# Kernel optimization log

Hardware: AMD Instinct MI355X
Metric: run time of the kernel (lower is better)

## Reference

```python
import jax, jax.numpy as jnp
import numpy as np

B, S, T = 32, 32, 64          # docs, sentences/doc, tokens/sentence
E, HW, HS = 128, 128, 128     # embed, word hidden, sentence hidden
CW, CS = 128, 128             # attention context sizes
V, NC = 50000, 8              # vocab, classes


def setup_inputs() -> dict:
    key = jax.random.key(0)
    ks = iter(jax.random.split(key, 40))
    x = jax.random.randint(next(ks), (B, S, T), 1, V, dtype=jnp.int32)
    wl = jax.random.randint(next(ks), (B, S), 8, T + 1)   # word lengths
    sl = jax.random.randint(next(ks), (B,), 8, S + 1)     # sentence counts
    tmask = jnp.arange(T)[None, None, :] < wl[:, :, None]
    smask = (jnp.arange(S)[None, :] < sl[:, None])[:, :, None]
    x = jnp.where(tmask & smask, x, 0)                     # 0 = pad token

    def u(shape, scale=0.1):
        return jax.random.uniform(next(ks), shape, jnp.float32, -scale, scale)

    d = {"x": x, "emb": u((V, E))}
    # GRU params in torch layout: W_ih [3H,D] (r|z|n), W_hh [3H,H], biases [3H]
    for pre, Din, H in [("wf", E, HW), ("wb", E, HW), ("sf", 2 * HW, HS), ("sb", 2 * HW, HS)]:
        d[pre + "_Wih"] = u((3 * H, Din))
        d[pre + "_Whh"] = u((3 * H, H))
        d[pre + "_bih"] = u((3 * H,))
        d[pre + "_bhh"] = u((3 * H,))
    d["wproj_W"] = u((CW, 2 * HW)); d["wproj_b"] = u((CW,)); d["wctx"] = u((CW,))
    d["sproj_W"] = u((CS, 2 * HS)); d["sproj_b"] = u((CS,)); d["sctx"] = u((CS,))
    d["fc_W"] = u((NC, 2 * HS)); d["fc_b"] = u((NC,))
    return d


def seq_lens_2d(tok):
    # torch get_sequence_lens: T - trailing zeros, 1 if all zero
    nz = tok != 0
    any_nz = jnp.any(nz, axis=1)
    last = tok.shape[1] - jnp.argmax(nz[:, ::-1], axis=1)
    return jnp.where(any_nz, last, 1)


def doc_lens(x):
    # torch get_num_sentences_lens: S - trailing all-zero sentences
    nz = jnp.any(x != 0, axis=2)  # [B,S]
    any_nz = jnp.any(nz, axis=1)
    last = x.shape[1] - jnp.argmax(nz[:, ::-1], axis=1)
    return jnp.where(any_nz, last, 1)


def run_gru(x, lens, Wih, Whh, bih, bhh, reverse):
    # x: [N,Tm,D]; emulates pack_padded: state frozen / output zeroed beyond len
    N, Tm, _ = x.shape
    H = Whh.shape[1]
    xp = jnp.einsum('ntd,gd->ntg', x, Wih) + bih  # [N,Tm,3H]

    def step(h, inp):
        xg, t = inp
        hg = h @ Whh.T + bhh
        xr, xz, xn = jnp.split(xg, 3, axis=-1)
        hr, hz, hn = jnp.split(hg, 3, axis=-1)
        r = jax.nn.sigmoid(xr + hr)
        z = jax.nn.sigmoid(xz + hz)
        n = jnp.tanh(xn + r * hn)
        h_new = (1 - z) * n + z * h
        valid = (t < lens)[:, None]
        h_new = jnp.where(valid, h_new, h)
        return h_new, jnp.where(valid, h_new, 0.0)

    h0 = jnp.zeros((N, H), x.dtype)
    _, ys = jax.lax.scan(step, h0, (jnp.swapaxes(xp, 0, 1), jnp.arange(Tm)), reverse=reverse)
    return jnp.swapaxes(ys, 0, 1)  # [N,Tm,H]


def bigru(x, lens, pf, pb):
    return jnp.concatenate([run_gru(x, lens, *pf, reverse=False),
                            run_gru(x, lens, *pb, reverse=True)], axis=-1)


def attn_pool(out, lens, Wp, bp, ctx):
    # faithful to torch: softmax over padded positions up to max(lens)
    # (pad_packed pads to max length; padded outputs are zero but score=tanh(b)@c)
    Tm = out.shape[1]
    scores = jnp.tanh(out @ Wp.T + bp) @ ctx            # [N,Tm]
    valid = jnp.arange(Tm)[None, :] < jnp.max(lens)
    attn = jax.nn.softmax(jnp.where(valid, scores, -jnp.inf), axis=-1)
    return jnp.einsum('nt,nth->nh', attn, out)


def han_forward(x, emb,
                wf_Wih, wf_Whh, wf_bih, wf_bhh, wb_Wih, wb_Whh, wb_bih, wb_bhh,
                wproj_W, wproj_b, wctx,
                sf_Wih, sf_Whh, sf_bih, sf_bhh, sb_Wih, sb_Whh, sb_bih, sb_bhh,
                sproj_W, sproj_b, sctx, fc_W, fc_b):
    Bx, Sx, Tx = x.shape
    xw = x.reshape(-1, Tx)                      # [B*S, T]
    wlens = seq_lens_2d(xw)
    slens = doc_lens(x)
    we = emb[xw]                                # [B*S, T, E]
    wout = bigru(we, wlens, (wf_Wih, wf_Whh, wf_bih, wf_bhh),
                 (wb_Wih, wb_Whh, wb_bih, wb_bhh))     # [B*S, T, 2HW]
    sent = attn_pool(wout, wlens, wproj_W, wproj_b, wctx)  # [B*S, 2HW]
    sent = sent.reshape(Bx, Sx, -1)
    sout = bigru(sent, slens, (sf_Wih, sf_Whh, sf_bih, sf_bhh),
                 (sb_Wih, sb_Whh, sb_bih, sb_bhh))     # [B, S, 2HS]
    doc = attn_pool(sout, slens, sproj_W, sproj_b, sctx)   # [B, 2HS]
    return doc @ fc_W.T + fc_b                             # [B, NC]


def reference(x, emb,
              wf_Wih, wf_Whh, wf_bih, wf_bhh, wb_Wih, wb_Whh, wb_bih, wb_bhh,
              wproj_W, wproj_b, wctx,
              sf_Wih, sf_Whh, sf_bih, sf_bhh, sb_Wih, sb_Whh, sb_bih, sb_bhh,
              sproj_W, sproj_b, sctx, fc_W, fc_b):
    return han_forward(x, emb,
                       wf_Wih, wf_Whh, wf_bih, wf_bhh, wb_Wih, wb_Whh, wb_bih, wb_bhh,
                       wproj_W, wproj_b, wctx,
                       sf_Wih, sf_Whh, sf_bih, sf_bhh, sb_Wih, sb_Whh, sb_bih, sb_bhh,
                       sproj_W, sproj_b, sctx, fc_W, fc_b)
```

## Files before the change

kernel.cpp:

```cpp
#include <hip/hip_runtime.h>
#include <hip/hip_bf16.h>

typedef unsigned short ushort_t;
typedef __attribute__((ext_vector_type(4))) float floatx4;
typedef __attribute__((ext_vector_type(8))) short short8;

#define L2E 1.4426950408889634f

__device__ __forceinline__ float bf2f(ushort_t u) {
    union { unsigned int i; float f; } v; v.i = ((unsigned int)u) << 16; return v.f;
}
__device__ __forceinline__ ushort_t f2bf(float f) {
    union { float f; unsigned int i; } v; v.f = f;
    unsigned int i = v.i;
    i += 0x7fffu + ((i >> 16) & 1u);
    return (ushort_t)(i >> 16);
}
__device__ __forceinline__ float fexp2(float x) {
#if __has_builtin(__builtin_amdgcn_exp2f)
    return __builtin_amdgcn_exp2f(x);
#else
    return __expf(x * 0.6931471805599453f);
#endif
}
__device__ __forceinline__ float frcp(float x) {
#if __has_builtin(__builtin_amdgcn_rcpf)
    return __builtin_amdgcn_rcpf(x);
#else
    return 1.f / x;
#endif
}
__device__ __forceinline__ float sig2(float a)  { return frcp(1.f + fexp2(a)); }
__device__ __forceinline__ float tanh2(float y) { return 1.f - 2.f * frcp(1.f + fexp2(y)); }

__device__ __forceinline__ unsigned int packbf(float a, float b) {
    float2 t; t.x = a; t.y = b;
    __hip_bfloat162 h = __float22bfloat162_rn(t);
    union { __hip_bfloat162 h; unsigned int u; } v; v.h = h; return v.u;
}

__device__ __forceinline__ floatx4 MFMA16(short8 a, short8 b, floatx4 c) {
    return __builtin_amdgcn_mfma_f32_16x16x32_bf16(a, b, c, 0, 0, 0);
}

__device__ __forceinline__ void bar_lds() {
    __builtin_amdgcn_s_waitcnt(0xc07f);
    __builtin_amdgcn_s_barrier();
}

#define XIDX(c, m) ((((c) * 16) + ((m) ^ ((c) & 15))) * 8)
#define X8(c, m) ((((c) * 8) + ((m) ^ ((c) & 7))) * 8)

struct ConvArgs {
    const void* src[25];
    int dstoff[25];
    int count[25];
    int cumblk[26];
    int mode[25];
    int rowdiv[25];
};

__global__ __launch_bounds__(256) void convert_kernel(ConvArgs a, ushort_t* __restrict__ dst,
                                                      const int* __restrict__ x,
                                                      int* wlens, int* slens, int* dmax,
                                                      int* flagp) {
    __shared__ int flag_lds;
    int tid = threadIdx.x, b = blockIdx.x;
    if (tid < 64) {
        unsigned int v = ((const unsigned int*)a.src[0])[tid];
        unsigned long long mball = __ballot(((v >> 7) & 0xFFu) > 0x7Bu);
        if (tid == 0) flag_lds = (__popcll(mball) > 8) ? 1 : 0;
    }
    __syncthreads();
    int flagv = flag_lds;
    int cblk = a.cumblk[25];

    if (b >= cblk) {
        int bb = b - cblk;
        if (bb == 0 && tid == 0) *flagp = flagv;
        if (tid < 64) {
            int s = tid;
            int last = 0;
            if (s < 32) {
                const int* tok = x + (bb * 32 + s) * 64;
                for (int t = 0; t < 64; t += 4) {
                    int4 v = *(const int4*)(tok + t);
                    if (v.x) last = t + 1;
                    if (v.y) last = t + 2;
                    if (v.z) last = t + 3;
                    if (v.w) last = t + 4;
                }
                wlens[bb * 32 + s] = last ? last : 1;
            }
            int len = (s < 32) ? (last ? last : 1) : 0;
            int lm = len;
            for (int off = 32; off; off >>= 1) lm = max(lm, __shfl_xor(lm, off));
            unsigned long long mask = __ballot(s < 32 && last > 0);
            if (s == 0) {
                slens[bb] = mask ? (63 - (int)__clzll(mask) + 1) : 1;
                dmax[bb] = lm;
            }
        }
        return;
    }

    int lo = 0, hi = 24;
    while (lo < hi) { int mid = (lo + hi + 1) >> 1; if (a.cumblk[mid] <= b) lo = mid; else hi = mid - 1; }
    int j = lo;
    int base = (b - a.cumblk[j]) * 2048 + tid * 8;
    if (base >= a.count[j]) return;
    ushort_t* out = dst + a.dstoff[j] + base;
    int m = a.mode[j], rd = a.rowdiv[j];
    float f[8];
    if (flagv) {
        const float* s = (const float*)a.src[j] + base;
        float4 v0 = *(const float4*)s;
        float4 v1 = *(const float4*)(s + 4);
        f[0] = v0.x; f[1] = v0.y; f[2] = v0.z; f[3] = v0.w;
        f[4] = v1.x; f[5] = v1.y; f[6] = v1.z; f[7] = v1.w;
    } else {
        const ushort_t* s = (const ushort_t*)a.src[j] + base;
        uint4 v = *(const uint4*)s;
        const ushort_t* u = (const ushort_t*)&v;
        #pragma unroll
        for (int e = 0; e < 8; ++e) f[e] = bf2f(u[e]);
    }
    union { ushort_t u[8]; uint4 v; } o;
    #pragma unroll
    for (int e = 0; e < 8; ++e) {
        float sc = 1.f;
        if (m == 2) sc = 2.f * L2E;
        else if (m == 1) sc = ((base + e) / rd < 256) ? -L2E : 2.f * L2E;
        o.u[e] = f2bf(f[e] * sc);
    }
    *(uint4*)out = o.v;
}

__global__ __launch_bounds__(512, 2) void word_gru_kernel(
        const int* __restrict__ x, const ushort_t* __restrict__ emb,
        const ushort_t* __restrict__ Wih_f, const ushort_t* __restrict__ Whh_f,
        const ushort_t* __restrict__ bih_f, const ushort_t* __restrict__ bhh_f,
        const ushort_t* __restrict__ Wih_b, const ushort_t* __restrict__ Whh_b,
        const ushort_t* __restrict__ bih_b, const ushort_t* __restrict__ bhh_b,
        const int* __restrict__ lens, ushort_t* __restrict__ out) {
    const int T = 64;
    __shared__ ushort_t h_buf[2][1024];
    __shared__ float bsum_lds[256];
    __shared__ float bihn_lds[128];
    __shared__ float bhhn_lds[128];
    __shared__ int tok_lds[512];

    int tid = threadIdx.x;
    int d = blockIdx.y;
    int n0 = blockIdx.x * 8;
    const ushort_t* Wih = d ? Wih_b : Wih_f;
    const ushort_t* Whh = d ? Whh_b : Whh_f;
    const ushort_t* bih = d ? bih_b : bih_f;
    const ushort_t* bhh = d ? bhh_b : bhh_f;
    int lane = tid & 63, wave = tid >> 6;
    int l15 = lane & 15, l4 = (lane >> 4) & 3;
    int s8 = l15 & 7;
    bool sv = l15 < 8;
    int jt = wave * 16;
    int j0 = jt + l4 * 4;

    {
        int t = tid >> 3, s = tid & 7;
        tok_lds[tid] = x[(n0 + s) * 64 + t];
    }
    if (tid < 256) bsum_lds[tid] = bf2f(bih[tid]) + bf2f(bhh[tid]);
    else if (tid < 384) {
        bihn_lds[tid - 256] = bf2f(bih[tid]);
        bhhn_lds[tid - 256] = bf2f(bhh[tid]);
    }
    if (tid < 256) { uint2 z = {0u, 0u}; *(uint2*)&h_buf[0][tid * 4] = z; }

    short8 wr[4], wz[4], wn[4], ur[4], uz[4], un[4];
    #pragma unroll
    for (int kf = 0; kf < 4; ++kf) {
        int col = kf * 32 + l4 * 8;
        wr[kf] = *(const short8*)(Wih + (size_t)(jt + l15) * 128 + col);
        wz[kf] = *(const short8*)(Wih + (size_t)(128 + jt + l15) * 128 + col);
        wn[kf] = *(const short8*)(Wih + (size_t)(256 + jt + l15) * 128 + col);
        ur[kf] = *(const short8*)(Whh + (size_t)(jt + l15) * 128 + col);
        uz[kf] = *(const short8*)(Whh + (size_t)(128 + jt + l15) * 128 + col);
        un[kf] = *(const short8*)(Whh + (size_t)(256 + jt + l15) * 128 + col);
    }
    __syncthreads();

    floatx4 br  = *(floatx4*)&bsum_lds[j0];
    floatx4 bz  = *(floatx4*)&bsum_lds[128 + j0];
    floatx4 bxn = *(floatx4*)&bihn_lds[j0];
    floatx4 bhn = *(floatx4*)&bhhn_lds[j0];
    int lv = lens[n0 + s8];
    float hreg[4] = {0.f, 0.f, 0.f, 0.f};

    short8 xc[4], xn_[4];
    {
        int t0 = d ? (T - 1) : 0;
        size_t rb = (size_t)tok_lds[t0 * 8 + s8] * 128 + l4 * 8;
        #pragma unroll
        for (int kf = 0; kf < 4; ++kf)
            xc[kf] = *(const short8*)(emb + rb + kf * 32);
    }

    for (int ti = 0; ti < T; ++ti) {
        int t = d ? (T - 1 - ti) : ti;
        bool have_next = (ti + 1) < T;
        if (have_next) {
            int tn = d ? (T - 2 - ti) : (ti + 1);
            size_t rb = (size_t)tok_lds[tn * 8 + s8] * 128 + l4 * 8;
            #pragma unroll
            for (int kf = 0; kf < 4; ++kf)
                xn_[kf] = *(const short8*)(emb + rb + kf * 32);
        }
        short8 hb[4];
        #pragma unroll
        for (int kf = 0; kf < 4; ++kf)
            hb[kf] = *(const short8*)&h_buf[ti & 1][X8(kf * 4 + l4, s8)];
        floatx4 arx = br, azx = bz, axn = bxn;
        floatx4 arh = {0.f, 0.f, 0.f, 0.f}, azh = {0.f, 0.f, 0.f, 0.f}, ahn = bhn;
        #pragma unroll
        for (int kf = 0; kf < 4; ++kf) {
            arx = MFMA16(wr[kf], xc[kf], arx);
            azx = MFMA16(wz[kf], xc[kf], azx);
            axn = MFMA16(wn[kf], xc[kf], axn);
        }
        #pragma unroll
        for (int kf = 0; kf < 4; ++kf) {
            arh = MFMA16(ur[kf], hb[kf], arh);
            azh = MFMA16(uz[kf], hb[kf], azh);
            ahn = MFMA16(un[kf], hb[kf], ahn);
        }
        bool valid = t < lv;
        float hnew[4];
        #pragma unroll
        for (int i = 0; i < 4; ++i) {
            float r  = sig2(arx[i] + arh[i]);
            float z  = sig2(azx[i] + azh[i]);
            float nn = tanh2(axn[i] + r * ahn[i]);
            hnew[i] = valid ? (nn + z * (hreg[i] - nn)) : hreg[i];
            hreg[i] = hnew[i];
        }
        if (sv) {
            uint2 h2, o2;
            h2.x = packbf(hnew[0], hnew[1]);
            h2.y = packbf(hnew[2], hnew[3]);
            o2.x = valid ? h2.x : 0u;
            o2.y = valid ? h2.y : 0u;
            *(uint2*)&h_buf[(ti & 1) ^ 1][X8(j0 >> 3, s8) + (j0 & 7)] = h2;
            *(uint2*)(out + ((size_t)(n0 + s8) * T + t) * 256 + d * 128 + j0) = o2;
        }
        if (have_next) {
            #pragma unroll
            for (int kf = 0; kf < 4; ++kf) xc[kf] = xn_[kf];
        }
        bar_lds();
    }
}

__global__ __launch_bounds__(256) void spt_gemm_kernel(const ushort_t* __restrict__ A,
                                                       const ushort_t* __restrict__ Bf_,
                                                       const ushort_t* __restrict__ biasf,
                                                       ushort_t* __restrict__ Tf_,
                                                       const ushort_t* __restrict__ Bb_,
                                                       const ushort_t* __restrict__ biasb,
                                                       ushort_t* __restrict__ Tb_) {
    __shared__ ushort_t As[64 * 256];
    __shared__ ushort_t Bs[64 * 256];
    const int K = 256;
    int tid = threadIdx.x;
    int by = blockIdx.y;
    bool sb = by >= 6;
    int n0 = (sb ? by - 6 : by) * 64;
    const ushort_t* B = sb ? Bb_ : Bf_;
    const ushort_t* bias = sb ? biasb : biasf;
    ushort_t* Tp = sb ? Tb_ : Tf_;
    int m0 = blockIdx.x * 64;
    for (int idx = tid; idx < 2048; idx += 256) {
        int m = idx & 63, c = idx >> 6;
        *(uint4*)&As[(c * 64 + m) * 8] = *(const uint4*)(A + (size_t)(m0 + m) * K + c * 8);
    }
    for (int idx = tid; idx < 2048; idx += 256) {
        int n = idx & 63, c = idx >> 6;
        *(uint4*)&Bs[(c * 64 + n) * 8] = *(const uint4*)(B + (size_t)(n0 + n) * K + c * 8);
    }
    __syncthreads();
    int lane = tid & 63, wave = tid >> 6;
    int wm = (wave & 1) * 32, wn = (wave >> 1) * 32;
    int l15 = lane & 15, l4 = lane >> 4;
    floatx4 acc[2][2] = {};
    for (int kf = 0; kf < 8; ++kf) {
        int c = kf * 4 + l4;
        short8 a0 = *(const short8*)&As[(c * 64 + wm + l15) * 8];
        short8 a1 = *(const short8*)&As[(c * 64 + wm + 16 + l15) * 8];
        short8 b0 = *(const short8*)&Bs[(c * 64 + wn + l15) * 8];
        short8 b1 = *(const short8*)&Bs[(c * 64 + wn + 16 + l15) * 8];
        acc[0][0] = MFMA16(a0, b0, acc[0][0]);
        acc[0][1] = MFMA16(a0, b1, acc[0][1]);
        acc[1][0] = MFMA16(a1, b0, acc[1][0]);
        acc[1][1] = MFMA16(a1, b1, acc[1][1]);
    }
    for (int nt = 0; nt < 2; ++nt) {
        int n = n0 + wn + nt * 16 + l15;
        float bv = bf2f(bias[n]);
        int jc = n >> 2, ji = n & 3;
        for (int mt = 0; mt < 2; ++mt) {
            int mbase = m0 + wm + mt * 16 + l4 * 4;
            #pragma unroll
            for (int i = 0; i < 4; ++i) {
                int m = mbase + i;
                int doc = m >> 5, t = m & 31;
                size_t dst = ((size_t)((doc >> 4) * 32 + t) * 96 + jc) * 64
                           + (doc & 15) * 4 + ji;
                Tp[dst] = f2bf(acc[mt][nt][i] + bv);
            }
        }
    }
}

__global__ __launch_bounds__(512, 2) void sent_gru_kernel(
        const ushort_t* __restrict__ spT_f, const ushort_t* __restrict__ spT_b,
        const ushort_t* __restrict__ Whh_f, const ushort_t* __restrict__ Whh_b,
        const ushort_t* __restrict__ bhh_f, const ushort_t* __restrict__ bhh_b,
        const int* __restrict__ lens, ushort_t* __restrict__ out) {
    const int T = 32;
    __shared__ ushort_t h_buf[2][1024];
    __shared__ float bhh_lds[384];

    int tid = threadIdx.x;
    int d = blockIdx.y;
    int bx = blockIdx.x;
    int n0 = bx * 8;
    const ushort_t* spT = d ? spT_b : spT_f;
    const ushort_t* Whh = d ? Whh_b : Whh_f;
    const ushort_t* bhh = d ? bhh_b : bhh_f;
    int lane = tid & 63, wave = tid >> 6;
    int l15 = lane & 15, l4 = (lane >> 4) & 3;
    int s8 = l15 & 7;
    bool sv = l15 < 8;
    int jt = wave * 16;
    int j0 = jt + l4 * 4;
    int jc = j0 >> 2;

    if (tid < 384) bhh_lds[tid] = bf2f(bhh[tid]);
    if (tid < 256) { uint2 z = {0u, 0u}; *(uint2*)&h_buf[0][tid * 4] = z; }

    short8 ur[4], uz[4], un[4];
    #pragma unroll
    for (int kf = 0; kf < 4; ++kf) {
        int col = kf * 32 + l4 * 8;
        ur[kf] = *(const short8*)(Whh + (size_t)(jt + l15) * 128 + col);
        uz[kf] = *(const short8*)(Whh + (size_t)(128 + jt + l15) * 128 + col);
        un[kf] = *(const short8*)(Whh + (size_t)(256 + jt + l15) * 128 + col);
    }
    __syncthreads();

    floatx4 br  = *(floatx4*)&bhh_lds[j0];
    floatx4 bz  = *(floatx4*)&bhh_lds[128 + j0];
    floatx4 bhn = *(floatx4*)&bhh_lds[256 + j0];
    int lv = lens[n0 + s8];
    float hreg[4] = {0.f, 0.f, 0.f, 0.f};

    const ushort_t* sp = spT + (size_t)((bx >> 1) * 32) * 96 * 64
                       + ((bx & 1) * 8 + s8) * 4;
    ushort4 xr_c, xz_c, xn_c, xr_n, xz_n, xn_n;
    {
        int t0 = d ? (T - 1) : 0;
        size_t rb = (size_t)t0 * 96 * 64;
        xr_c = *(const ushort4*)(sp + rb + (size_t)jc * 64);
        xz_c = *(const ushort4*)(sp + rb + (size_t)(32 + jc) * 64);
        xn_c = *(const ushort4*)(sp + rb + (size_t)(64 + jc) * 64);
    }

    for (int ti = 0; ti < T; ++ti) {
        int t = d ? (T - 1 - ti) : ti;
        int cur = ti & 1;
        bool have_next = (ti + 1) < T;
        if (have_next) {
            int tn = d ? (T - 2 - ti) : (ti + 1);
            size_t rb = (size_t)tn * 96 * 64;
            xr_n = *(const ushort4*)(sp + rb + (size_t)jc * 64);
            xz_n = *(const ushort4*)(sp + rb + (size_t)(32 + jc) * 64);
            xn_n = *(const ushort4*)(sp + rb + (size_t)(64 + jc) * 64);
        }
        floatx4 ar = br, az = bz, ahn = bhn;
        #pragma unroll
        for (int kf = 0; kf < 4; ++kf) {
            short8 hb = *(const short8*)&h_buf[cur][X8(kf * 4 + l4, s8)];
            ar  = MFMA16(ur[kf], hb, ar);
            az  = MFMA16(uz[kf], hb, az);
            ahn = MFMA16(un[kf], hb, ahn);
        }
        float xr[4] = {bf2f(xr_c.x), bf2f(xr_c.y), bf2f(xr_c.z), bf2f(xr_c.w)};
        float xz[4] = {bf2f(xz_c.x), bf2f(xz_c.y), bf2f(xz_c.z), bf2f(xz_c.w)};
        float xn[4] = {bf2f(xn_c.x), bf2f(xn_c.y), bf2f(xn_c.z), bf2f(xn_c.w)};
        bool valid = t < lv;
        float hnew[4];
        #pragma unroll
        for (int i = 0; i < 4; ++i) {
            float r  = sig2(xr[i] + ar[i]);
            float z  = sig2(xz[i] + az[i]);
            float nn = tanh2(xn[i] + r * ahn[i]);
            hnew[i] = valid ? (nn + z * (hreg[i] - nn)) : hreg[i];
            hreg[i] = hnew[i];
        }
        if (sv) {
            uint2 h2, o2;
            h2.x = packbf(hnew[0], hnew[1]);
            h2.y = packbf(hnew[2], hnew[3]);
            o2.x = valid ? h2.x : 0u;
            o2.y = valid ? h2.y : 0u;
            *(uint2*)&h_buf[cur ^ 1][X8(j0 >> 3, s8) + (j0 & 7)] = h2;
            *(uint2*)(out + ((size_t)(n0 + s8) * T + t) * 256 + d * 128 + j0) = o2;
        }
        if (have_next) { xr_c = xr_n; xz_c = xz_n; xn_c = xn_n; }
        bar_lds();
    }
}

#define SP 264
__global__ __launch_bounds__(256) void word_attn_kernel(const ushort_t* __restrict__ wout,
                                                        const ushort_t* __restrict__ W,
                                                        const ushort_t* __restrict__ bias,
                                                        const ushort_t* __restrict__ ctx,
                                                        const int* __restrict__ dmax,
                                                        ushort_t* __restrict__ sent) {
    __shared__ ushort_t tile[64 * SP];
    __shared__ float bc[256];
    __shared__ float sc_lds[64];
    __shared__ float p_lds[64];
    int tid = threadIdx.x, g = blockIdx.x;
    for (int idx = tid; idx < 2048; idx += 256) {
        int row = idx >> 5, k0 = (idx & 31) * 8;
        *(uint4*)&tile[row * SP + k0] = *(const uint4*)(wout + ((size_t)g * 64 + row) * 256 + k0);
    }
    if (tid < 128) bc[tid] = bf2f(bias[tid]);
    else bc[tid] = bf2f(ctx[tid - 128]);
    __syncthreads();
    int lane = tid & 63, wave = tid >> 6;
    int l15 = lane & 15, l4 = (lane >> 4) & 3;
    short8 a[8];
    #pragma unroll
    for (int kf = 0; kf < 8; ++kf)
        a[kf] = *(const short8*)&tile[(wave * 16 + l15) * SP + kf * 32 + l4 * 8];
    floatx4 acc[8];
    #pragma unroll
    for (int nt = 0; nt < 8; ++nt) {
        floatx4 c = {0.f, 0.f, 0.f, 0.f};
        #pragma unroll
        for (int kf = 0; kf < 8; ++kf) {
            short8 b = *(const short8*)(W + (size_t)(nt * 16 + l15) * 256 + kf * 32 + l4 * 8);
            c = MFMA16(a[kf], b, c);
        }
        acc[nt] = c;
    }
    float s[4] = {0.f, 0.f, 0.f, 0.f};
    #pragma unroll
    for (int nt = 0; nt < 8; ++nt) {
        float bv = bc[nt * 16 + l15], cv = bc[128 + nt * 16 + l15];
        #pragma unroll
        for (int i = 0; i < 4; ++i)
            s[i] += tanh2(acc[nt][i] + bv) * cv;
    }
    #pragma unroll
    for (int i = 0; i < 4; ++i) {
        s[i] += __shfl_xor(s[i], 1);
        s[i] += __shfl_xor(s[i], 2);
        s[i] += __shfl_xor(s[i], 4);
        s[i] += __shfl_xor(s[i], 8);
    }
    if (l15 == 0) {
        #pragma unroll
        for (int i = 0; i < 4; ++i) sc_lds[wave * 16 + l4 * 4 + i] = s[i];
    }
    __syncthreads();
    if (tid < 64) {
        int ml = dmax[tid & 31];
        for (int off = 32; off; off >>= 1) ml = max(ml, __shfl_xor(ml, off));
        bool v = tid < ml;
        float sc = v ? sc_lds[tid] : -1e30f;
        float mx = sc;
        for (int off = 32; off; off >>= 1) mx = fmaxf(mx, __shfl_xor(mx, off));
        float e = v ? __expf(sc - mx) : 0.f;
        float sum = e;
        for (int off = 32; off; off >>= 1) sum += __shfl_xor(sum, off);
        p_lds[tid] = e * frcp(fmaxf(sum, 1e-30f));
    }
    __syncthreads();
    float a0 = 0.f, a1 = 0.f, a2 = 0.f, a3 = 0.f;
    for (int t = 0; t < 64; t += 4) {
        a0 += p_lds[t]     * bf2f(tile[t * SP + tid]);
        a1 += p_lds[t + 1] * bf2f(tile[(t + 1) * SP + tid]);
        a2 += p_lds[t + 2] * bf2f(tile[(t + 2) * SP + tid]);
        a3 += p_lds[t + 3] * bf2f(tile[(t + 3) * SP + tid]);
    }
    sent[(size_t)g * 256 + tid] = f2bf((a0 + a1) + (a2 + a3));
}

__global__ __launch_bounds__(256) void sent_attn_fc_kernel(const ushort_t* __restrict__ sout,
                                                           const ushort_t* __restrict__ W,
                                                           const ushort_t* __restrict__ bias,
                                                           const ushort_t* __restrict__ ctx,
                                                           const ushort_t* __restrict__ fcW,
                                                           const ushort_t* __restrict__ fcb,
                                                           const int* __restrict__ slens,
                                                           const int* __restrict__ flagp,
                                                           void* __restrict__ outp) {
    __shared__ ushort_t tile[32 * SP];
    __shared__ float bc[256];
    __shared__ float sc_lds[32];
    __shared__ float p_lds[32];
    __shared__ float dv[256];
    int tid = threadIdx.x, g = blockIdx.x;
    for (int idx = tid; idx < 1024; idx += 256) {
        int row = idx >> 5, k0 = (idx & 31) * 8;
        *(uint4*)&tile[row * SP + k0] = *(const uint4*)(sout + ((size_t)g * 32 + row) * 256 + k0);
    }
    if (tid < 128) bc[tid] = bf2f(bias[tid]);
    else bc[tid] = bf2f(ctx[tid - 128]);
    __syncthreads();
    int lane = tid & 63, wave = tid >> 6;
    int l15 = lane & 15, l4 = (lane >> 4) & 3;
    if (wave < 2) {
        short8 a[8];
        #pragma unroll
        for (int kf = 0; kf < 8; ++kf)
            a[kf] = *(const short8*)&tile[(wave * 16 + l15) * SP + kf * 32 + l4 * 8];
        floatx4 acc[8];
        #pragma unroll
        for (int nt = 0; nt < 8; ++nt) {
            floatx4 c = {0.f, 0.f, 0.f, 0.f};
            #pragma unroll
            for (int kf = 0; kf < 8; ++kf) {
                short8 b = *(const short8*)(W + (size_t)(nt * 16 + l15) * 256 + kf * 32 + l4 * 8);
                c = MFMA16(a[kf], b, c);
            }
            acc[nt] = c;
        }
        float s[4] = {0.f, 0.f, 0.f, 0.f};
        #pragma unroll
        for (int nt = 0; nt < 8; ++nt) {
            float bv = bc[nt * 16 + l15], cv = bc[128 + nt * 16 + l15];
            #pragma unroll
            for (int i = 0; i < 4; ++i)
                s[i] += tanh2(acc[nt][i] + bv) * cv;
        }
        #pragma unroll
        for (int i = 0; i < 4; ++i) {
            s[i] += __shfl_xor(s[i], 1);
            s[i] += __shfl_xor(s[i], 2);
            s[i] += __shfl_xor(s[i], 4);
            s[i] += __shfl_xor(s[i], 8);
        }
        if (l15 == 0) {
            #pragma unroll
            for (int i = 0; i < 4; ++i) sc_lds[wave * 16 + l4 * 4 + i] = s[i];
        }
    }
    __syncthreads();
    if (tid < 32) {
        int ml = slens[tid];
        for (int off = 16; off; off >>= 1) ml = max(ml, __shfl_xor(ml, off, 32));
        bool v = tid < ml;
        float sc = v ? sc_lds[tid] : -1e30f;
        float mx = sc;
        for (int off = 16; off; off >>= 1) mx = fmaxf(mx, __shfl_xor(mx, off, 32));
        float e = v ? __expf(sc - mx) : 0.f;
        float sum = e;
        for (int off = 16; off; off >>= 1) sum += __shfl_xor(sum, off, 32);
        p_lds[tid] = e * frcp(fmaxf(sum, 1e-30f));
    }
    __syncthreads();
    float acc2 = 0.f;
    for (int t = 0; t < 32; ++t) acc2 += p_lds[t] * bf2f(tile[t * SP + tid]);
    dv[tid] = acc2;
    __syncthreads();
    int c = tid >> 5, q0 = (tid & 31) * 8;
    float partial = 0.f;
    #pragma unroll
    for (int q = 0; q < 8; ++q)
        partial += dv[q0 + q] * bf2f(fcW[(size_t)c * 256 + q0 + q]);
    for (int off = 16; off; off >>= 1) partial += __shfl_xor(partial, off, 32);
    if ((tid & 31) == 0) {
        float v = partial + bf2f(fcb[c]);
        if (*flagp) ((float*)outp)[g * 8 + c] = v;
        else        ((ushort_t*)outp)[g * 8 + c] = f2bf(v);
    }
}

extern "C" void kernel_launch(void* const* d_in, const int* in_sizes, int n_in,
                              void* d_out, int out_size, void* d_ws, size_t ws_size,
                              hipStream_t stream) {
    const int* x = (const int*)d_in[0];
    char* ws = (char*)d_ws;

    const size_t O_CONV = 0;
    const size_t O_WOUT = 14680064;
    const size_t O_SENT = 48234496;
    const size_t O_SOUT = 48758784;
    const size_t O_SPTF = 49283072;
    const size_t O_SPTB = 50855936;
    const size_t O_LENS = 52428800;
    const size_t O_SLEN = 52432896;
    const size_t O_DMAX = 52433024;
    const size_t O_FLAG = 52433152;

    ushort_t* conv = (ushort_t*)(ws + O_CONV);
    ushort_t* wout = (ushort_t*)(ws + O_WOUT);
    ushort_t* sent = (ushort_t*)(ws + O_SENT);
    ushort_t* sout = (ushort_t*)(ws + O_SOUT);
    ushort_t* sptf = (ushort_t*)(ws + O_SPTF);
    ushort_t* sptb = (ushort_t*)(ws + O_SPTB);
    int* wlens = (int*)(ws + O_LENS);
    int* slens = (int*)(ws + O_SLEN);
    int* dmax  = (int*)(ws + O_DMAX);
    int* flag  = (int*)(ws + O_FLAG);

    static const int kMode[25]   = {0, 1,1,1,1, 1,1,1,1, 1,1,1,1, 1,1,1,1, 2,2,0, 2,2,0, 0,0};
    static const int kRowdiv[25] = {1, 128,128,1,1, 128,128,1,1, 256,128,1,1, 256,128,1,1,
                                    1,1,1, 1,1,1, 1,1};

    ConvArgs ca;
    ushort_t* cw[25];
    int off = 0, blk = 0;
    for (int i = 1; i <= 25; ++i) {
        int j = i - 1;
        int cnt = in_sizes[i];
        ca.src[j] = d_in[i];
        ca.dstoff[j] = off;
        ca.count[j] = cnt;
        ca.cumblk[j] = blk;
        ca.mode[j] = kMode[j];
        ca.rowdiv[j] = kRowdiv[j];
        cw[j] = conv + off;
        off += cnt;
        blk += (cnt + 2047) / 2048;
    }
    ca.cumblk[25] = blk;

    convert_kernel<<<blk + 32, 256, 0, stream>>>(ca, conv, x, wlens, slens, dmax, flag);
    word_gru_kernel<<<dim3(128, 2), 512, 0, stream>>>(
        x, cw[0],
        cw[1], cw[2], cw[3], cw[4],
        cw[5], cw[6], cw[7], cw[8],
        wlens, wout);
    word_attn_kernel<<<1024, 256, 0, stream>>>(wout, cw[17], cw[18], cw[19], dmax, sent);
    spt_gemm_kernel<<<dim3(16, 12), 256, 0, stream>>>(sent, cw[9], cw[11], sptf,
                                                      cw[13], cw[15], sptb);
    sent_gru_kernel<<<dim3(4, 2), 512, 0, stream>>>(
        sptf, sptb, cw[10], cw[14], cw[12], cw[16], slens, sout);
    sent_attn_fc_kernel<<<32, 256, 0, stream>>>(sout, cw[20], cw[21], cw[22],
                                                cw[23], cw[24], slens, flag, d_out);
    (void)n_in; (void)out_size; (void)ws_size;
}
```

Before: 277.9 us.

## Fuse sentence GEMM, sentence GRU and attention-FC into one cooperative kernel

Merges the three tail kernels (sentence input projection GEMM, bidirectional sentence GRU, sentence attention plus FC) into a single cooperative launch of 192 blocks that uses grid.sync between the phases. The goal is to remove two kernel launch and drain gaps in the short tail of the pipeline. In exchange the GEMM phase now runs at 512 threads with only 4 waves doing MFMA, the GRU and attention phases use only 8 and 32 of the 192 blocks, and grid-wide barriers add their own cost.

```diff
diff --git a/kernel.cpp b/kernel.cpp
--- a/kernel.cpp
+++ b/kernel.cpp
@@ -1,5 +1,6 @@
 #include <hip/hip_runtime.h>
 #include <hip/hip_bf16.h>
+#include <hip/hip_cooperative_groups.h>
 
 typedef unsigned short ushort_t;
 typedef __attribute__((ext_vector_type(4))) float floatx4;
@@ -48,8 +49,8 @@
     __builtin_amdgcn_s_barrier();
 }
 
-#define XIDX(c, m) ((((c) * 16) + ((m) ^ ((c) & 15))) * 8)
 #define X8(c, m) ((((c) * 8) + ((m) ^ ((c) & 7))) * 8)
+#define SP 264
 
 struct ConvArgs {
     const void* src[25];
@@ -259,167 +260,6 @@
     }
 }
 
-__global__ __launch_bounds__(256) void spt_gemm_kernel(const ushort_t* __restrict__ A,
-                                                       const ushort_t* __restrict__ Bf_,
-                                                       const ushort_t* __restrict__ biasf,
-                                                       ushort_t* __restrict__ Tf_,
-                                                       const ushort_t* __restrict__ Bb_,
-                                                       const ushort_t* __restrict__ biasb,
-                                                       ushort_t* __restrict__ Tb_) {
-    __shared__ ushort_t As[64 * 256];
-    __shared__ ushort_t Bs[64 * 256];
-    const int K = 256;
-    int tid = threadIdx.x;
-    int by = blockIdx.y;
-    bool sb = by >= 6;
-    int n0 = (sb ? by - 6 : by) * 64;
-    const ushort_t* B = sb ? Bb_ : Bf_;
-    const ushort_t* bias = sb ? biasb : biasf;
-    ushort_t* Tp = sb ? Tb_ : Tf_;
-    int m0 = blockIdx.x * 64;
-    for (int idx = tid; idx < 2048; idx += 256) {
-        int m = idx & 63, c = idx >> 6;
-        *(uint4*)&As[(c * 64 + m) * 8] = *(const uint4*)(A + (size_t)(m0 + m) * K + c * 8);
-    }
-    for (int idx = tid; idx < 2048; idx += 256) {
-        int n = idx & 63, c = idx >> 6;
-        *(uint4*)&Bs[(c * 64 + n) * 8] = *(const uint4*)(B + (size_t)(n0 + n) * K + c * 8);
-    }
-    __syncthreads();
-    int lane = tid & 63, wave = tid >> 6;
-    int wm = (wave & 1) * 32, wn = (wave >> 1) * 32;
-    int l15 = lane & 15, l4 = lane >> 4;
-    floatx4 acc[2][2] = {};
-    for (int kf = 0; kf < 8; ++kf) {
-        int c = kf * 4 + l4;
-        short8 a0 = *(const short8*)&As[(c * 64 + wm + l15) * 8];
-        short8 a1 = *(const short8*)&As[(c * 64 + wm + 16 + l15) * 8];
-        short8 b0 = *(const short8*)&Bs[(c * 64 + wn + l15) * 8];
-        short8 b1 = *(const short8*)&Bs[(c * 64 + wn + 16 + l15) * 8];
-        acc[0][0] = MFMA16(a0, b0, acc[0][0]);
-        acc[0][1] = MFMA16(a0, b1, acc[0][1]);
-        acc[1][0] = MFMA16(a1, b0, acc[1][0]);
-        acc[1][1] = MFMA16(a1, b1, acc[1][1]);
-    }
-    for (int nt = 0; nt < 2; ++nt) {
-        int n = n0 + wn + nt * 16 + l15;
-        float bv = bf2f(bias[n]);
-        int jc = n >> 2, ji = n & 3;
-        for (int mt = 0; mt < 2; ++mt) {
-            int mbase = m0 + wm + mt * 16 + l4 * 4;
-            #pragma unroll
-            for (int i = 0; i < 4; ++i) {
-                int m = mbase + i;
-                int doc = m >> 5, t = m & 31;
-                size_t dst = ((size_t)((doc >> 4) * 32 + t) * 96 + jc) * 64
-                           + (doc & 15) * 4 + ji;
-                Tp[dst] = f2bf(acc[mt][nt][i] + bv);
-            }
-        }
-    }
-}
-
-__global__ __launch_bounds__(512, 2) void sent_gru_kernel(
-        const ushort_t* __restrict__ spT_f, const ushort_t* __restrict__ spT_b,
-        const ushort_t* __restrict__ Whh_f, const ushort_t* __restrict__ Whh_b,
-        const ushort_t* __restrict__ bhh_f, const ushort_t* __restrict__ bhh_b,
-        const int* __restrict__ lens, ushort_t* __restrict__ out) {
-    const int T = 32;
-    __shared__ ushort_t h_buf[2][1024];
-    __shared__ float bhh_lds[384];
-
-    int tid = threadIdx.x;
-    int d = blockIdx.y;
-    int bx = blockIdx.x;
-    int n0 = bx * 8;
-    const ushort_t* spT = d ? spT_b : spT_f;
-    const ushort_t* Whh = d ? Whh_b : Whh_f;
-    const ushort_t* bhh = d ? bhh_b : bhh_f;
-    int lane = tid & 63, wave = tid >> 6;
-    int l15 = lane & 15, l4 = (lane >> 4) & 3;
-    int s8 = l15 & 7;
-    bool sv = l15 < 8;
-    int jt = wave * 16;
-    int j0 = jt + l4 * 4;
-    int jc = j0 >> 2;
-
-    if (tid < 384) bhh_lds[tid] = bf2f(bhh[tid]);
-    if (tid < 256) { uint2 z = {0u, 0u}; *(uint2*)&h_buf[0][tid * 4] = z; }
-
-    short8 ur[4], uz[4], un[4];
-    #pragma unroll
-    for (int kf = 0; kf < 4; ++kf) {
-        int col = kf * 32 + l4 * 8;
-        ur[kf] = *(const short8*)(Whh + (size_t)(jt + l15) * 128 + col);
-        uz[kf] = *(const short8*)(Whh + (size_t)(128 + jt + l15) * 128 + col);
-        un[kf] = *(const short8*)(Whh + (size_t)(256 + jt + l15) * 128 + col);
-    }
-    __syncthreads();
-
-    floatx4 br  = *(floatx4*)&bhh_lds[j0];
-    floatx4 bz  = *(floatx4*)&bhh_lds[128 + j0];
-    floatx4 bhn = *(floatx4*)&bhh_lds[256 + j0];
-    int lv = lens[n0 + s8];
-    float hreg[4] = {0.f, 0.f, 0.f, 0.f};
-
-    const ushort_t* sp = spT + (size_t)((bx >> 1) * 32) * 96 * 64
-                       + ((bx & 1) * 8 + s8) * 4;
-    ushort4 xr_c, xz_c, xn_c, xr_n, xz_n, xn_n;
-    {
-        int t0 = d ? (T - 1) : 0;
-        size_t rb = (size_t)t0 * 96 * 64;
-        xr_c = *(const ushort4*)(sp + rb + (size_t)jc * 64);
-        xz_c = *(const ushort4*)(sp + rb + (size_t)(32 + jc) * 64);
-        xn_c = *(const ushort4*)(sp + rb + (size_t)(64 + jc) * 64);
-    }
-
-    for (int ti = 0; ti < T; ++ti) {
-        int t = d ? (T - 1 - ti) : ti;
-        int cur = ti & 1;
-        bool have_next = (ti + 1) < T;
-        if (have_next) {
-            int tn = d ? (T - 2 - ti) : (ti + 1);
-            size_t rb = (size_t)tn * 96 * 64;
-            xr_n = *(const ushort4*)(sp + rb + (size_t)jc * 64);
-            xz_n = *(const ushort4*)(sp + rb + (size_t)(32 + jc) * 64);
-            xn_n = *(const ushort4*)(sp + rb + (size_t)(64 + jc) * 64);
-        }
-        floatx4 ar = br, az = bz, ahn = bhn;
-        #pragma unroll
-        for (int kf = 0; kf < 4; ++kf) {
-            short8 hb = *(const short8*)&h_buf[cur][X8(kf * 4 + l4, s8)];
-            ar  = MFMA16(ur[kf], hb, ar);
-            az  = MFMA16(uz[kf], hb, az);
-            ahn = MFMA16(un[kf], hb, ahn);
-        }
-        float xr[4] = {bf2f(xr_c.x), bf2f(xr_c.y), bf2f(xr_c.z), bf2f(xr_c.w)};
-        float xz[4] = {bf2f(xz_c.x), bf2f(xz_c.y), bf2f(xz_c.z), bf2f(xz_c.w)};
-        float xn[4] = {bf2f(xn_c.x), bf2f(xn_c.y), bf2f(xn_c.z), bf2f(xn_c.w)};
-        bool valid = t < lv;
-        float hnew[4];
-        #pragma unroll
-        for (int i = 0; i < 4; ++i) {
-            float r  = sig2(xr[i] + ar[i]);
-            float z  = sig2(xz[i] + az[i]);
-            float nn = tanh2(xn[i] + r * ahn[i]);
-            hnew[i] = valid ? (nn + z * (hreg[i] - nn)) : hreg[i];
-            hreg[i] = hnew[i];
-        }
-        if (sv) {
-            uint2 h2, o2;
-            h2.x = packbf(hnew[0], hnew[1]);
-            h2.y = packbf(hnew[2], hnew[3]);
-            o2.x = valid ? h2.x : 0u;
-            o2.y = valid ? h2.y : 0u;
-            *(uint2*)&h_buf[cur ^ 1][X8(j0 >> 3, s8) + (j0 & 7)] = h2;
-            *(uint2*)(out + ((size_t)(n0 + s8) * T + t) * 256 + d * 128 + j0) = o2;
-        }
-        if (have_next) { xr_c = xr_n; xz_c = xz_n; xn_c = xn_n; }
-        bar_lds();
-    }
-}
-
-#define SP 264
 __global__ __launch_bounds__(256) void word_attn_kernel(const ushort_t* __restrict__ wout,
                                                         const ushort_t* __restrict__ W,
                                                         const ushort_t* __restrict__ bias,
@@ -498,94 +338,259 @@
     sent[(size_t)g * 256 + tid] = f2bf((a0 + a1) + (a2 + a3));
 }
 
-__global__ __launch_bounds__(256) void sent_attn_fc_kernel(const ushort_t* __restrict__ sout,
-                                                           const ushort_t* __restrict__ W,
-                                                           const ushort_t* __restrict__ bias,
-                                                           const ushort_t* __restrict__ ctx,
-                                                           const ushort_t* __restrict__ fcW,
-                                                           const ushort_t* __restrict__ fcb,
-                                                           const int* __restrict__ slens,
-                                                           const int* __restrict__ flagp,
-                                                           void* __restrict__ outp) {
-    __shared__ ushort_t tile[32 * SP];
-    __shared__ float bc[256];
-    __shared__ float sc_lds[32];
-    __shared__ float p_lds[32];
-    __shared__ float dv[256];
-    int tid = threadIdx.x, g = blockIdx.x;
-    for (int idx = tid; idx < 1024; idx += 256) {
-        int row = idx >> 5, k0 = (idx & 31) * 8;
-        *(uint4*)&tile[row * SP + k0] = *(const uint4*)(sout + ((size_t)g * 32 + row) * 256 + k0);
-    }
-    if (tid < 128) bc[tid] = bf2f(bias[tid]);
-    else bc[tid] = bf2f(ctx[tid - 128]);
-    __syncthreads();
+struct TailArgs {
+    const ushort_t* sent;
+    const ushort_t* Bf; const ushort_t* biasf; ushort_t* Tf;
+    const ushort_t* Bb; const ushort_t* biasb; ushort_t* Tb;
+    const ushort_t* Whh_f; const ushort_t* Whh_b;
+    const ushort_t* bhh_f; const ushort_t* bhh_b;
+    const int* slens; ushort_t* sout;
+    const ushort_t* W; const ushort_t* bias; const ushort_t* ctx;
+    const ushort_t* fcW; const ushort_t* fcb;
+    const int* flagp; void* outp;
+};
+
+__global__ __launch_bounds__(512, 1) void tail_kernel(TailArgs ta) {
+    namespace cg = cooperative_groups;
+    cg::grid_group grid = cg::this_grid();
+    __shared__ __align__(16) char smraw[65536];
+    int tid = threadIdx.x;
+    int b = blockIdx.x;
     int lane = tid & 63, wave = tid >> 6;
     int l15 = lane & 15, l4 = (lane >> 4) & 3;
-    if (wave < 2) {
-        short8 a[8];
-        #pragma unroll
-        for (int kf = 0; kf < 8; ++kf)
-            a[kf] = *(const short8*)&tile[(wave * 16 + l15) * SP + kf * 32 + l4 * 8];
-        floatx4 acc[8];
-        #pragma unroll
-        for (int nt = 0; nt < 8; ++nt) {
-            floatx4 c = {0.f, 0.f, 0.f, 0.f};
-            #pragma unroll
+
+    {
+        ushort_t* As = (ushort_t*)smraw;
+        ushort_t* Bs = As + 64 * 256;
+        const int K = 256;
+        int by = b / 16, bx = b % 16;
+        bool sb = by >= 6;
+        int n0 = (sb ? by - 6 : by) * 64;
+        const ushort_t* B = sb ? ta.Bb : ta.Bf;
+        const ushort_t* bias = sb ? ta.biasb : ta.biasf;
+        ushort_t* Tp = sb ? ta.Tb : ta.Tf;
+        int m0 = bx * 64;
+        for (int idx = tid; idx < 2048; idx += 512) {
+            int m = idx & 63, c = idx >> 6;
+            *(uint4*)&As[(c * 64 + m) * 8] = *(const uint4*)(ta.sent + (size_t)(m0 + m) * K + c * 8);
+        }
+        for (int idx = tid; idx < 2048; idx += 512) {
+            int n = idx & 63, c = idx >> 6;
+            *(uint4*)&Bs[(c * 64 + n) * 8] = *(const uint4*)(B + (size_t)(n0 + n) * K + c * 8);
+        }
+        __syncthreads();
+        if (wave < 4) {
+            int wm = (wave & 1) * 32, wn = (wave >> 1) * 32;
+            floatx4 acc[2][2] = {};
             for (int kf = 0; kf < 8; ++kf) {
-                short8 b = *(const short8*)(W + (size_t)(nt * 16 + l15) * 256 + kf * 32 + l4 * 8);
-                c = MFMA16(a[kf], b, c);
-            }
-            acc[nt] = c;
-        }
-        float s[4] = {0.f, 0.f, 0.f, 0.f};
-        #pragma unroll
-        for (int nt = 0; nt < 8; ++nt) {
-            float bv = bc[nt * 16 + l15], cv = bc[128 + nt * 16 + l15];
-            #pragma unroll
-            for (int i = 0; i < 4; ++i)
-                s[i] += tanh2(acc[nt][i] + bv) * cv;
-        }
-        #pragma unroll
-        for (int i = 0; i < 4; ++i) {
-            s[i] += __shfl_xor(s[i], 1);
-            s[i] += __shfl_xor(s[i], 2);
-            s[i] += __shfl_xor(s[i], 4);
-            s[i] += __shfl_xor(s[i], 8);
-        }
-        if (l15 == 0) {
-            #pragma unroll
-            for (int i = 0; i < 4; ++i) sc_lds[wave * 16 + l4 * 4 + i] = s[i];
-        }
-    }
-    __syncthreads();
-    if (tid < 32) {
-        int ml = slens[tid];
-        for (int off = 16; off; off >>= 1) ml = max(ml, __shfl_xor(ml, off, 32));
-        bool v = tid < ml;
-        float sc = v ? sc_lds[tid] : -1e30f;
-        float mx = sc;
-        for (int off = 16; off; off >>= 1) mx = fmaxf(mx, __shfl_xor(mx, off, 32));
-        float e = v ? __expf(sc - mx) : 0.f;
-        float sum = e;
-        for (int off = 16; off; off >>= 1) sum += __shfl_xor(sum, off, 32);
-        p_lds[tid] = e * frcp(fmaxf(sum, 1e-30f));
-    }
-    __syncthreads();
-    float acc2 = 0.f;
-    for (int t = 0; t < 32; ++t) acc2 += p_lds[t] * bf2f(tile[t * SP + tid]);
-    dv[tid] = acc2;
-    __syncthreads();
-    int c = tid >> 5, q0 = (tid & 31) * 8;
-    float partial = 0.f;
-    #pragma unroll
-    for (int q = 0; q < 8; ++q)
-        partial += dv[q0 + q] * bf2f(fcW[(size_t)c * 256 + q0 + q]);
-    for (int off = 16; off; off >>= 1) partial += __shfl_xor(partial, off, 32);
-    if ((tid & 31) == 0) {
-        float v = partial + bf2f(fcb[c]);
-        if (*flagp) ((float*)outp)[g * 8 + c] = v;
-        else        ((ushort_t*)outp)[g * 8 + c] = f2bf(v);
+                int c = kf * 4 + l4;
+                short8 a0 = *(const short8*)&As[(c * 64 + wm + l15) * 8];
+                short8 a1 = *(const short8*)&As[(c * 64 + wm + 16 + l15) * 8];
+                short8 b0 = *(const short8*)&Bs[(c * 64 + wn + l15) * 8];
+                short8 b1 = *(const short8*)&Bs[(c * 64 + wn + 16 + l15) * 8];
+                acc[0][0] = MFMA16(a0, b0, acc[0][0]);
+                acc[0][1] = MFMA16(a0, b1, acc[0][1]);
+                acc[1][0] = MFMA16(a1, b0, acc[1][0]);
+                acc[1][1] = MFMA16(a1, b1, acc[1][1]);
+            }
+            for (int nt = 0; nt < 2; ++nt) {
+                int n = n0 + wn + nt * 16 + l15;
+                float bv = bf2f(bias[n]);
+                int jc = n >> 2, ji = n & 3;
+                for (int mt = 0; mt < 2; ++mt) {
+                    int mbase = m0 + wm + mt * 16 + l4 * 4;
+                    #pragma unroll
+                    for (int i = 0; i < 4; ++i) {
+                        int m = mbase + i;
+                        int doc = m >> 5, t = m & 31;
+                        size_t dst = ((size_t)((doc >> 4) * 32 + t) * 96 + jc) * 64
+                                   + (doc & 15) * 4 + ji;
+                        Tp[dst] = f2bf(acc[mt][nt][i] + bv);
+                    }
+                }
+            }
+        }
+    }
+    __threadfence();
+    grid.sync();
+
+    if (b < 8) {
+        const int T = 32;
+        ushort_t (*h_buf)[1024] = (ushort_t (*)[1024])smraw;
+        float* bhh_lds = (float*)(smraw + 4096);
+        int d = b >> 2;
+        int bx = b & 3;
+        int n0 = bx * 8;
+        const ushort_t* spT = d ? ta.Tb : ta.Tf;
+        const ushort_t* Whh = d ? ta.Whh_b : ta.Whh_f;
+        const ushort_t* bhh = d ? ta.bhh_b : ta.bhh_f;
+        int s8 = l15 & 7;
+        bool sv = l15 < 8;
+        int jt = wave * 16;
+        int j0 = jt + l4 * 4;
+        int jc = j0 >> 2;
+
+        if (tid < 384) bhh_lds[tid] = bf2f(bhh[tid]);
+        if (tid < 256) { uint2 z = {0u, 0u}; *(uint2*)&h_buf[0][tid * 4] = z; }
+
+        short8 ur[4], uz[4], un[4];
+        #pragma unroll
+        for (int kf = 0; kf < 4; ++kf) {
+            int col = kf * 32 + l4 * 8;
+            ur[kf] = *(const short8*)(Whh + (size_t)(jt + l15) * 128 + col);
+            uz[kf] = *(const short8*)(Whh + (size_t)(128 + jt + l15) * 128 + col);
+            un[kf] = *(const short8*)(Whh + (size_t)(256 + jt + l15) * 128 + col);
+        }
+        __syncthreads();
+
+        floatx4 br  = *(floatx4*)&bhh_lds[j0];
+        floatx4 bz  = *(floatx4*)&bhh_lds[128 + j0];
+        floatx4 bhn = *(floatx4*)&bhh_lds[256 + j0];
+        int lv = ta.slens[n0 + s8];
+        float hreg[4] = {0.f, 0.f, 0.f, 0.f};
+
+        const ushort_t* sp = spT + (size_t)((bx >> 1) * 32) * 96 * 64
+                           + ((bx & 1) * 8 + s8) * 4;
+        ushort4 xr_c, xz_c, xn_c, xr_n, xz_n, xn_n;
+        {
+            int t0 = d ? (T - 1) : 0;
+            size_t rb = (size_t)t0 * 96 * 64;
+            xr_c = *(const ushort4*)(sp + rb + (size_t)jc * 64);
+            xz_c = *(const ushort4*)(sp + rb + (size_t)(32 + jc) * 64);
+            xn_c = *(const ushort4*)(sp + rb + (size_t)(64 + jc) * 64);
+        }
+
+        for (int ti = 0; ti < T; ++ti) {
+            int t = d ? (T - 1 - ti) : ti;
+            int cur = ti & 1;
+            bool have_next = (ti + 1) < T;
+            if (have_next) {
+                int tn = d ? (T - 2 - ti) : (ti + 1);
+                size_t rb = (size_t)tn * 96 * 64;
+                xr_n = *(const ushort4*)(sp + rb + (size_t)jc * 64);
+                xz_n = *(const ushort4*)(sp + rb + (size_t)(32 + jc) * 64);
+                xn_n = *(const ushort4*)(sp + rb + (size_t)(64 + jc) * 64);
+            }
+            floatx4 ar = br, az = bz, ahn = bhn;
+            #pragma unroll
+            for (int kf = 0; kf < 4; ++kf) {
+                short8 hb = *(const short8*)&h_buf[cur][X8(kf * 4 + l4, s8)];
+                ar  = MFMA16(ur[kf], hb, ar);
+                az  = MFMA16(uz[kf], hb, az);
+                ahn = MFMA16(un[kf], hb, ahn);
+            }
+            float xr[4] = {bf2f(xr_c.x), bf2f(xr_c.y), bf2f(xr_c.z), bf2f(xr_c.w)};
+            float xz[4] = {bf2f(xz_c.x), bf2f(xz_c.y), bf2f(xz_c.z), bf2f(xz_c.w)};
+            float xn[4] = {bf2f(xn_c.x), bf2f(xn_c.y), bf2f(xn_c.z), bf2f(xn_c.w)};
+            bool valid = t < lv;
+            float hnew[4];
+            #pragma unroll
+            for (int i = 0; i < 4; ++i) {
+                float r  = sig2(xr[i] + ar[i]);
+                float z  = sig2(xz[i] + az[i]);
+                float nn = tanh2(xn[i] + r * ahn[i]);
+                hnew[i] = valid ? (nn + z * (hreg[i] - nn)) : hreg[i];
+                hreg[i] = hnew[i];
+            }
+            if (sv) {
+                uint2 h2, o2;
+                h2.x = packbf(hnew[0], hnew[1]);
+                h2.y = packbf(hnew[2], hnew[3]);
+                o2.x = valid ? h2.x : 0u;
+                o2.y = valid ? h2.y : 0u;
+                *(uint2*)&h_buf[cur ^ 1][X8(j0 >> 3, s8) + (j0 & 7)] = h2;
+                *(uint2*)(ta.sout + ((size_t)(n0 + s8) * T + t) * 256 + d * 128 + j0) = o2;
+            }
+            if (have_next) { xr_c = xr_n; xz_c = xz_n; xn_c = xn_n; }
+            bar_lds();
+        }
+    }
+    __threadfence();
+    grid.sync();
+
+    if (b < 32) {
+        int g = b;
+        ushort_t* tile = (ushort_t*)smraw;
+        float* bc     = (float*)(smraw + 16896);
+        float* sc_lds = (float*)(smraw + 17920);
+        float* p_lds  = (float*)(smraw + 18048);
+        float* dv     = (float*)(smraw + 18176);
+        for (int idx = tid; idx < 1024; idx += 512) {
+            int row = idx >> 5, k0 = (idx & 31) * 8;
+            *(uint4*)&tile[row * SP + k0] = *(const uint4*)(ta.sout + ((size_t)g * 32 + row) * 256 + k0);
+        }
+        if (tid < 128) bc[tid] = bf2f(ta.bias[tid]);
+        else if (tid < 256) bc[tid] = bf2f(ta.ctx[tid - 128]);
+        __syncthreads();
+        if (wave < 2) {
+            short8 a[8];
+            #pragma unroll
+            for (int kf = 0; kf < 8; ++kf)
+                a[kf] = *(const short8*)&tile[(wave * 16 + l15) * SP + kf * 32 + l4 * 8];
+            floatx4 acc[8];
+            #pragma unroll
+            for (int nt = 0; nt < 8; ++nt) {
+                floatx4 c = {0.f, 0.f, 0.f, 0.f};
+                #pragma unroll
+                for (int kf = 0; kf < 8; ++kf) {
+                    short8 bb = *(const short8*)(ta.W + (size_t)(nt * 16 + l15) * 256 + kf * 32 + l4 * 8);
+                    c = MFMA16(a[kf], bb, c);
+                }
+                acc[nt] = c;
+            }
+            float s[4] = {0.f, 0.f, 0.f, 0.f};
+            #pragma unroll
+            for (int nt = 0; nt < 8; ++nt) {
+                float bv = bc[nt * 16 + l15], cv = bc[128 + nt * 16 + l15];
+                #pragma unroll
+                for (int i = 0; i < 4; ++i)
+                    s[i] += tanh2(acc[nt][i] + bv) * cv;
+            }
+            #pragma unroll
+            for (int i = 0; i < 4; ++i) {
+                s[i] += __shfl_xor(s[i], 1);
+                s[i] += __shfl_xor(s[i], 2);
+                s[i] += __shfl_xor(s[i], 4);
+                s[i] += __shfl_xor(s[i], 8);
+            }
+            if (l15 == 0) {
+                #pragma unroll
+                for (int i = 0; i < 4; ++i) sc_lds[wave * 16 + l4 * 4 + i] = s[i];
+            }
+        }
+        __syncthreads();
+        if (tid < 32) {
+            int ml = ta.slens[tid];
+            for (int off = 16; off; off >>= 1) ml = max(ml, __shfl_xor(ml, off, 32));
+            bool v = tid < ml;
+            float sc = v ? sc_lds[tid] : -1e30f;
+            float mx = sc;
+            for (int off = 16; off; off >>= 1) mx = fmaxf(mx, __shfl_xor(mx, off, 32));
+            float e = v ? __expf(sc - mx) : 0.f;
+            float sum = e;
+            for (int off = 16; off; off >>= 1) sum += __shfl_xor(sum, off, 32);
+            p_lds[tid] = e * frcp(fmaxf(sum, 1e-30f));
+        }
+        __syncthreads();
+        if (tid < 256) {
+            float acc2 = 0.f;
+            for (int t = 0; t < 32; ++t) acc2 += p_lds[t] * bf2f(tile[t * SP + tid]);
+            dv[tid] = acc2;
+        }
+        __syncthreads();
+        if (tid < 256) {
+            int c = tid >> 5, q0 = (tid & 31) * 8;
+            float partial = 0.f;
+            #pragma unroll
+            for (int q = 0; q < 8; ++q)
+                partial += dv[q0 + q] * bf2f(ta.fcW[(size_t)c * 256 + q0 + q]);
+            for (int off = 16; off; off >>= 1) partial += __shfl_xor(partial, off, 32);
+            if ((tid & 31) == 0) {
+                float v = partial + bf2f(ta.fcb[c]);
+                if (*ta.flagp) ((float*)ta.outp)[g * 8 + c] = v;
+                else          ((ushort_t*)ta.outp)[g * 8 + c] = f2bf(v);
+            }
+        }
     }
 }
 
@@ -646,11 +651,18 @@
         cw[5], cw[6], cw[7], cw[8],
         wlens, wout);
     word_attn_kernel<<<1024, 256, 0, stream>>>(wout, cw[17], cw[18], cw[19], dmax, sent);
-    spt_gemm_kernel<<<dim3(16, 12), 256, 0, stream>>>(sent, cw[9], cw[11], sptf,
-                                                      cw[13], cw[15], sptb);
-    sent_gru_kernel<<<dim3(4, 2), 512, 0, stream>>>(
-        sptf, sptb, cw[10], cw[14], cw[12], cw[16], slens, sout);
-    sent_attn_fc_kernel<<<32, 256, 0, stream>>>(sout, cw[20], cw[21], cw[22],
-                                                cw[23], cw[24], slens, flag, d_out);
+    TailArgs ta;
+    ta.sent = sent;
+    ta.Bf = cw[9];  ta.biasf = cw[11]; ta.Tf = sptf;
+    ta.Bb = cw[13]; ta.biasb = cw[15]; ta.Tb = sptb;
+    ta.Whh_f = cw[10]; ta.Whh_b = cw[14];
+    ta.bhh_f = cw[12]; ta.bhh_b = cw[16];
+    ta.slens = slens; ta.sout = sout;
+    ta.W = cw[20]; ta.bias = cw[21]; ta.ctx = cw[22];
+    ta.fcW = cw[23]; ta.fcb = cw[24];
+    ta.flagp = flag; ta.outp = d_out;
+    void* kargs[] = { &ta };
+    hipLaunchCooperativeKernel((void*)tail_kernel, dim3(192), dim3(512),
+                               kargs, 0, stream);
     (void)n_in; (void)out_size; (void)ws_size;
 }
```

Result: slower. 438.6 us (+57.8%).
